# Kernel tuning notes

Measured on AMD Instinct MI355X. Metric: run time of the kernel, lower is better.

Reference implementation:

```python
import jax, jax.numpy as jnp
import numpy as np

VOCAB = 50257
D_MODEL = 1024
PAD_IDX = 0
B, L = 4, 4096


def setup_inputs() -> dict:
    key = jax.random.key(0)
    k_emb, k_R, k_ids, k_role = jax.random.split(key, 4)
    emb = jax.random.normal(k_emb, (VOCAB, D_MODEL), dtype=jnp.float32)
    emb = emb.at[PAD_IDX].set(0.0)  # nn.Embedding padding_idx row is zero
    R = jax.random.normal(k_R, (D_MODEL, D_MODEL), dtype=jnp.float32)
    input_ids = jax.random.randint(k_ids, (B, L), 0, VOCAB, dtype=jnp.int64)
    role_mask = jax.random.randint(k_role, (B, L), 0, 2, dtype=jnp.int64)
    return {"input_ids": input_ids, "role_mask": role_mask, "emb": emb, "R": R}


def reference(input_ids, role_mask, emb, R):
    # embedding gather: (B, L, D)
    x = emb[input_ids]
    # agent tokens get x @ R.T, user tokens pass through
    agent = (role_mask == 1)[..., None]
    transformed = jnp.einsum('bld,ed->ble', x, R)
    return jnp.where(agent, transformed, x)
```

## Files before the change

### kernel.cpp

```cpp
#include <hip/hip_runtime.h>
#include <hip/hip_bf16.h>
#include <stdint.h>

#define DMODEL 1024
#define M_TOK  16384

typedef __attribute__((ext_vector_type(8))) short short8;
typedef __attribute__((ext_vector_type(4))) float f32x4;

__device__ __forceinline__ unsigned int pack2_bf16(float f0, float f1) {
    unsigned int u0 = __builtin_bit_cast(unsigned int, f0);
    unsigned int u1 = __builtin_bit_cast(unsigned int, f1);
    u0 += 0x7fffu + ((u0 >> 16) & 1u);
    u1 += 0x7fffu + ((u1 >> 16) & 1u);
    return __builtin_amdgcn_perm(u1, u0, 0x07060302);
}

__device__ __forceinline__ void gload_lds16(const void* g, void* l) {
    __builtin_amdgcn_global_load_lds(
        (const __attribute__((address_space(1))) void*)g,
        (__attribute__((address_space(3))) void*)l, 16, 0, 0);
}

__global__ void zero_ctr(int* __restrict__ n_agent) { *n_agent = 0; }

__global__ void __launch_bounds__(1024)
gather3(const int* __restrict__ ids, const int* __restrict__ roles,
        const float* __restrict__ emb, const float* __restrict__ Rm,
        __hip_bfloat16* __restrict__ Xc, __hip_bfloat16* __restrict__ Rb,
        float* __restrict__ out, int* __restrict__ orig,
        int* __restrict__ n_agent) {
    __shared__ int s_cnt[16];
    __shared__ int s_slot[16];
    const int wave = threadIdx.x >> 6;
    const int lane = threadIdx.x & 63;
    const int blk  = blockIdx.x;
    if (blk < M_TOK / 16) {
        const int row  = blk * 16 + wave;
        const int id   = ids[row];
        const int role = roles[row];
        if (lane == 0) s_cnt[wave] = (role == 1);
        __syncthreads();
        if (threadIdx.x == 0) {
            int tot = 0, pre[16];
#pragma unroll
            for (int w = 0; w < 16; ++w) { pre[w] = tot; tot += s_cnt[w]; }
            const int base = atomicAdd(n_agent, tot);
#pragma unroll
            for (int w = 0; w < 16; ++w) s_slot[w] = base + pre[w];
        }
        __syncthreads();
        const float* src = emb + (size_t)id * DMODEL;
        if (role == 1) {
            const int slot = s_slot[wave];
            if (lane == 0) orig[slot] = row;
            unsigned short* dst = (unsigned short*)(Xc + (size_t)slot * DMODEL);
#pragma unroll
            for (int c = 0; c < 4; ++c) {
                const int idx = c * 256 + lane * 4;
                float4 v = *(const float4*)(src + idx);
                uint2 p = make_uint2(pack2_bf16(v.x, v.y), pack2_bf16(v.z, v.w));
                *(uint2*)(dst + idx) = p;
            }
        } else {
            float* dst = out + (size_t)row * DMODEL;
#pragma unroll
            for (int c = 0; c < 4; ++c) {
                const int idx = c * 256 + lane * 4;
                *(float4*)(dst + idx) = *(const float4*)(src + idx);
            }
        }
    } else {
        const int r = (blk - M_TOK / 16) * 16 + wave;
        const float* src = Rm + (size_t)r * DMODEL;
        unsigned short* dst = (unsigned short*)(Rb + (size_t)r * DMODEL);
#pragma unroll
        for (int c = 0; c < 4; ++c) {
            const int idx = c * 256 + lane * 4;
            float4 v = *(const float4*)(src + idx);
            uint2 p = make_uint2(pack2_bf16(v.x, v.y), pack2_bf16(v.z, v.w));
            *(uint2*)(dst + idx) = p;
        }
    }
}

__global__ void __launch_bounds__(256)
rse_gemm5(const int* __restrict__ n_agent_p, const int* __restrict__ orig,
          const __hip_bfloat16* __restrict__ Xc,
          const __hip_bfloat16* __restrict__ Rb,
          float* __restrict__ out) {
    const int na = *n_agent_p;
    const int m0 = blockIdx.x * 64;
    if (m0 >= na) return;
    const int n0 = blockIdx.y * 128;

    __shared__ __hip_bfloat16 As[2][64 * 64];
    __shared__ __hip_bfloat16 Bs[2][128 * 64];
    __shared__ int s_orig[64];

    const int tid  = threadIdx.x;
    const int lane = tid & 63;
    const int wave = tid >> 6;
    const int quad = lane >> 4;
    const int l15  = lane & 15;
    const int wr   = wave >> 1;
    const int wc   = wave & 1;

    if (tid < 64) {
        const int j = m0 + tid;
        s_orig[tid] = (j < na) ? orig[j] : -1;
    }

    const int st_row = lane >> 3;
    const int st_k   = ((lane & 7) ^ st_row) * 8;
    const __hip_bfloat16* aG = Xc + (size_t)m0 * DMODEL + st_k;
    const __hip_bfloat16* bG = Rb + (size_t)n0 * DMODEL + st_k;

#define STAGE(buf, k0)                                                        \
    do {                                                                      \
        _Pragma("unroll")                                                     \
        for (int q = 0; q < 2; ++q) {         \
            const int rg = (q * 4 + wave) * 8;                                \
            gload_lds16(aG + (size_t)(rg + st_row) * DMODEL + (k0),           \
                        &As[buf][rg * 64]);                                   \
        }                                                                     \
        _Pragma("unroll")                                                     \
        for (int q = 0; q < 4; ++q) {        \
            const int rg = (q * 4 + wave) * 8;                                \
            gload_lds16(bG + (size_t)(rg + st_row) * DMODEL + (k0),           \
                        &Bs[buf][rg * 64]);                                   \
        }                                                                     \
    } while (0)

    f32x4 acc[2][4] = {};

#define COMPUTE(buf)                                                          \
    do {                                                                      \
        _Pragma("unroll")                                                     \
        for (int kk = 0; kk < 2; ++kk) {                                      \
            short8 af[2], bfr[4];                                             \
            _Pragma("unroll")                                                 \
            for (int i = 0; i < 2; ++i) {                                     \
                const int r = wr * 32 + i * 16 + l15;                         \
                af[i] = *(const short8*)                                      \
                    &As[buf][r * 64 + ((kk * 4 + quad) ^ (r & 7)) * 8];       \
            }                                                                 \
            _Pragma("unroll")                                                 \
            for (int j = 0; j < 4; ++j) {                                     \
                const int r = wc * 64 + j * 16 + l15;                         \
                bfr[j] = *(const short8*)                                     \
                    &Bs[buf][r * 64 + ((kk * 4 + quad) ^ (r & 7)) * 8];       \
            }                                                                 \
            _Pragma("unroll")                                                 \
            for (int i = 0; i < 2; ++i)                                       \
                _Pragma("unroll")                                             \
                for (int j = 0; j < 4; ++j)                                   \
                    acc[i][j] = __builtin_amdgcn_mfma_f32_16x16x32_bf16(      \
                        af[i], bfr[j], acc[i][j], 0, 0, 0);                   \
        }                                                                     \
    } while (0)

    STAGE(0, 0);
    __syncthreads();

    for (int k0 = 0; k0 < DMODEL; k0 += 128) {
        STAGE(1, k0 + 64);
        COMPUTE(0);
        __syncthreads();
        if (k0 + 128 < DMODEL) STAGE(0, k0 + 128);
        COMPUTE(1);
        __syncthreads();
    }
#undef STAGE
#undef COMPUTE

    const int colbase = n0 + wc * 64 + l15;
#pragma unroll
    for (int i = 0; i < 2; ++i) {
        const int rowb = wr * 32 + i * 16 + quad * 4;
#pragma unroll
        for (int r = 0; r < 4; ++r) {
            const int oj = s_orig[rowb + r];
            if (oj >= 0) {
                float* dst = out + (size_t)oj * DMODEL + colbase;
#pragma unroll
                for (int j = 0; j < 4; ++j)
                    dst[j * 16] = acc[i][j][r];
            }
        }
    }
}

extern "C" void kernel_launch(void* const* d_in, const int* in_sizes, int n_in,
                              void* d_out, int out_size, void* d_ws, size_t ws_size,
                              hipStream_t stream) {
    const int*   ids   = (const int*)d_in[0];
    const int*   roles = (const int*)d_in[1];
    const float* emb   = (const float*)d_in[2];
    const float* Rm    = (const float*)d_in[3];
    float*       out   = (float*)d_out;

    __hip_bfloat16* Xc = (__hip_bfloat16*)d_ws;
    __hip_bfloat16* Rb = Xc + (size_t)M_TOK * DMODEL;
    int* orig    = (int*)(Rb + (size_t)DMODEL * DMODEL);
    int* n_agent = orig + M_TOK;

    zero_ctr<<<1, 1, 0, stream>>>(n_agent);
    gather3<<<M_TOK / 16 + DMODEL / 16, 1024, 0, stream>>>(
        ids, roles, emb, Rm, Xc, Rb, out, orig, n_agent);
    dim3 grid2(M_TOK / 64, DMODEL / 128);
    rse_gemm5<<<grid2, 256, 0, stream>>>(n_agent, orig, Xc, Rb, out);
}
```

Baseline: 314.8 us.

## Enlarge GEMM tile to 128x128 and hand-pipeline double-buffered LDS loads

The agent-row GEMM now uses 128x128 output tiles with a 4x4 MFMA accumulator grid per wave, doubling A-tile reuse and halving the number of blocks. The K loop is fully unrolled with explicit vmcnt/lgkmcnt waits and raw s_barrier, so two stages of global-to-LDS loads stay in flight while computing. The goal is more arithmetic per byte loaded and fewer full syncthreads stalls. The cost is more registers and LDS per block and fewer blocks to fill the GPU. The hand-written wait counts must match the number of outstanding loads exactly.

Result: no change. 316.7 us (+0.6%).

```diff
diff --git a/kernel.cpp b/kernel.cpp
--- a/kernel.cpp
+++ b/kernel.cpp
@@ -85,18 +85,18 @@
 }
 
 __global__ void __launch_bounds__(256)
-rse_gemm5(const int* __restrict__ n_agent_p, const int* __restrict__ orig,
+rse_gemm6(const int* __restrict__ n_agent_p, const int* __restrict__ orig,
           const __hip_bfloat16* __restrict__ Xc,
           const __hip_bfloat16* __restrict__ Rb,
           float* __restrict__ out) {
     const int na = *n_agent_p;
-    const int m0 = blockIdx.x * 64;
+    const int m0 = blockIdx.x * 128;
     if (m0 >= na) return;
     const int n0 = blockIdx.y * 128;
 
-    __shared__ __hip_bfloat16 As[2][64 * 64];
+    __shared__ __hip_bfloat16 As[2][128 * 64];
     __shared__ __hip_bfloat16 Bs[2][128 * 64];
-    __shared__ int s_orig[64];
+    __shared__ int s_orig[128];
 
     const int tid  = threadIdx.x;
     const int lane = tid & 63;
@@ -106,7 +106,7 @@
     const int wr   = wave >> 1;
     const int wc   = wave & 1;
 
-    if (tid < 64) {
+    if (tid < 128) {
         const int j = m0 + tid;
         s_orig[tid] = (j < na) ? orig[j] : -1;
     }
@@ -119,7 +119,7 @@
 #define STAGE(buf, k0)                                                        \
     do {                                                                      \
         _Pragma("unroll")                                                     \
-        for (int q = 0; q < 2; ++q) {         \
+        for (int q = 0; q < 4; ++q) {        \
             const int rg = (q * 4 + wave) * 8;                                \
             gload_lds16(aG + (size_t)(rg + st_row) * DMODEL + (k0),           \
                         &As[buf][rg * 64]);                                   \
@@ -132,16 +132,16 @@
         }                                                                     \
     } while (0)
 
-    f32x4 acc[2][4] = {};
+    f32x4 acc[4][4] = {};
 
 #define COMPUTE(buf)                                                          \
     do {                                                                      \
         _Pragma("unroll")                                                     \
         for (int kk = 0; kk < 2; ++kk) {                                      \
-            short8 af[2], bfr[4];                                             \
+            short8 af[4], bfr[4];                                             \
             _Pragma("unroll")                                                 \
-            for (int i = 0; i < 2; ++i) {                                     \
-                const int r = wr * 32 + i * 16 + l15;                         \
+            for (int i = 0; i < 4; ++i) {                                     \
+                const int r = wr * 64 + i * 16 + l15;                         \
                 af[i] = *(const short8*)                                      \
                     &As[buf][r * 64 + ((kk * 4 + quad) ^ (r & 7)) * 8];       \
             }                                                                 \
@@ -152,7 +152,7 @@
                     &Bs[buf][r * 64 + ((kk * 4 + quad) ^ (r & 7)) * 8];       \
             }                                                                 \
             _Pragma("unroll")                                                 \
-            for (int i = 0; i < 2; ++i)                                       \
+            for (int i = 0; i < 4; ++i)                                       \
                 _Pragma("unroll")                                             \
                 for (int j = 0; j < 4; ++j)                                   \
                     acc[i][j] = __builtin_amdgcn_mfma_f32_16x16x32_bf16(      \
@@ -161,31 +161,40 @@
     } while (0)
 
     STAGE(0, 0);
-    __syncthreads();
-
-    for (int k0 = 0; k0 < DMODEL; k0 += 128) {
-        STAGE(1, k0 + 64);
-        COMPUTE(0);
-        __syncthreads();
-        if (k0 + 128 < DMODEL) STAGE(0, k0 + 128);
-        COMPUTE(1);
-        __syncthreads();
+    STAGE(1, 64);
+
+#pragma unroll
+    for (int t = 0; t < 16; ++t) {
+        if (t == 0)
+            asm volatile("s_waitcnt vmcnt(8) lgkmcnt(0)" ::: "memory");
+        else if (t < 15)
+            asm volatile("s_waitcnt vmcnt(8)" ::: "memory");
+        else
+            asm volatile("s_waitcnt vmcnt(0)" ::: "memory");
+        __builtin_amdgcn_s_barrier();
+        COMPUTE(t & 1);
+        if (t < 14) {
+            asm volatile("s_waitcnt lgkmcnt(0)" ::: "memory");
+            __builtin_amdgcn_sched_barrier(0);
+            __builtin_amdgcn_s_barrier();
+            STAGE(t & 1, (t + 2) * 64);
+        }
     }
 #undef STAGE
 #undef COMPUTE
 
     const int colbase = n0 + wc * 64 + l15;
 #pragma unroll
-    for (int i = 0; i < 2; ++i) {
-        const int rowb = wr * 32 + i * 16 + quad * 4;
+    for (int ti = 0; ti < 4; ++ti) {
+        const int rowb = wr * 64 + ti * 16 + quad * 4;
 #pragma unroll
         for (int r = 0; r < 4; ++r) {
             const int oj = s_orig[rowb + r];
             if (oj >= 0) {
                 float* dst = out + (size_t)oj * DMODEL + colbase;
 #pragma unroll
-                for (int j = 0; j < 4; ++j)
-                    dst[j * 16] = acc[i][j][r];
+                for (int tj = 0; tj < 4; ++tj)
+                    dst[tj * 16] = acc[ti][tj][r];
             }
         }
     }
@@ -208,6 +217,6 @@
     zero_ctr<<<1, 1, 0, stream>>>(n_agent);
     gather3<<<M_TOK / 16 + DMODEL / 16, 1024, 0, stream>>>(
         ids, roles, emb, Rm, Xc, Rb, out, orig, n_agent);
-    dim3 grid2(M_TOK / 64, DMODEL / 128);
-    rse_gemm5<<<grid2, 256, 0, stream>>>(n_agent, orig, Xc, Rb, out);
-}
+    dim3 grid2(M_TOK / 128, DMODEL / 128);
+    rse_gemm6<<<grid2, 256, 0, stream>>>(n_agent, orig, Xc, Rb, out);
+}
```
